# Kernel tuning notes

Hardware: AMD Instinct MI355X
Metric: run time of the kernel (lower is better)

Reference implementation:

```python
import jax, jax.numpy as jnp
import numpy as np

NOISE_WEIGHT = 1.0
CHAMFER_WEIGHT = 0.1
CHUNK = 1024


def _min_dist_chunked(a, b):
    """For each point in a [B,N,3], squared distance to nearest point in b [B,M,3].
    Processed in chunks of CHUNK points of `a` to avoid materializing [B,N,M].
    Returns [B,N]."""
    B, N, _ = a.shape
    b_sq = jnp.sum(b * b, axis=-1)  # [B,M]
    nc = N // CHUNK
    a_chunks = jnp.moveaxis(a.reshape(B, nc, CHUNK, 3), 1, 0)  # [nc,B,CHUNK,3]

    def body(carry, a_c):
        a_sq = jnp.sum(a_c * a_c, axis=-1)  # [B,CHUNK]
        # d[b,i,j] = |a_i|^2 + |b_j|^2 - 2 a_i.b_j
        d = a_sq[:, :, None] + b_sq[:, None, :] - 2.0 * jnp.einsum('bid,bjd->bij', a_c, b)
        d = jnp.maximum(d, 0.0)
        return carry, jnp.min(d, axis=2)  # [B,CHUNK]

    _, mins = jax.lax.scan(body, None, a_chunks)  # [nc,B,CHUNK]
    return jnp.moveaxis(mins, 0, 1).reshape(B, N)


def chamfer_distance(pred, target):
    d_pt = _min_dist_chunked(pred, target)   # [B,N]
    d_tp = _min_dist_chunked(target, pred)   # [B,M]
    return jnp.mean(d_pt, axis=1) + jnp.mean(d_tp, axis=1)  # [B]


def setup_inputs() -> dict:
    key = jax.random.key(0)
    k1, k2, k3, k4 = jax.random.split(key, 4)
    B, N = 8, 16384
    return {
        'predicted_noise': jax.random.normal(k1, (B, N, 3), dtype=jnp.float32),
        'actual_noise': jax.random.normal(k2, (B, N, 3), dtype=jnp.float32),
        'predicted_points_coarse': jax.random.normal(k3, (B, N, 3), dtype=jnp.float32),
        'target_points_coarse': jax.random.normal(k4, (B, N, 3), dtype=jnp.float32),
    }


def reference(predicted_noise, actual_noise, predicted_points_coarse, target_points_coarse):
    noise_loss = jnp.mean(jnp.abs(predicted_noise - actual_noise))
    chamfer_loss = jnp.mean(chamfer_distance(predicted_points_coarse, target_points_coarse))
    total_loss = NOISE_WEIGHT * noise_loss + CHAMFER_WEIGHT * chamfer_loss
    return total_loss
```

## Files before the change

kernel.cpp:

```cpp
#include <hip/hip_runtime.h>
#include <stdint.h>

#define NPTS        16384
#define BATCH       8
#define QPB         128
#define QBLKS       (NPTS / QPB)
#define CHAM_BLOCKS (BATCH * 2 * QBLKS)
#define NOISE_N     (BATCH * NPTS * 3)
#define NOISE_V4    (NOISE_N / 4)
#define NPTS_TOT    (BATCH * NPTS)
#define PACK_BLOCKS (NPTS_TOT / 256)
#define REF_ITERS   (NPTS * 8 / 1024)

#define WS_NOISE_PART 0
#define WS_CHAM_PART  4096
#define WS_PK_PRED    16384
#define WS_PK_TARG    (WS_PK_PRED + 8 * NPTS_TOT)
#define WS_R_PRED     (WS_PK_TARG + 8 * NPTS_TOT)
#define WS_R_TARG     (WS_R_PRED + 4 * NPTS_TOT)

using halfx4 = __attribute__((ext_vector_type(4))) _Float16;
using intx4  = __attribute__((ext_vector_type(4))) int;

__device__ __forceinline__ unsigned int f2h(float f) {
  union { _Float16 h; unsigned short s; } v; v.h = (_Float16)f; return v.s;
}
__device__ __forceinline__ float h2f(unsigned short s) {
  union { _Float16 h; unsigned short u; } v; v.u = s; return (float)v.h;
}

__device__ __forceinline__ void mfma_min(halfx4 a, halfx4 b, float& acc) {
  asm("v_mfma_f32_32x32x8_f16 v[48:63], %1, %2, 0\n\t"
      "s_nop 7\n\t"
      "s_nop 7\n\t"
      "s_nop 1\n\t"
      "v_min3_f32 v48, v48, v49, v50\n\t"
      "v_min3_f32 v51, v51, v52, v53\n\t"
      "v_min3_f32 v54, v54, v55, v56\n\t"
      "v_min3_f32 v57, v57, v58, v59\n\t"
      "v_min3_f32 v60, v60, v61, v62\n\t"
      "v_min3_f32 v48, v48, v51, v54\n\t"
      "v_min3_f32 v57, v57, v60, v63\n\t"
      "v_min3_f32 %0, %0, v48, v57"
      : "+v"(acc)
      : "v"(a), "v"(b)
      : "v48","v49","v50","v51","v52","v53","v54","v55",
        "v56","v57","v58","v59","v60","v61","v62","v63");
}

__global__ void pack_noise_kernel(const float* __restrict__ pred,
                                  const float* __restrict__ targ,
                                  const float4* __restrict__ na,
                                  const float4* __restrict__ nb,
                                  ushort4* __restrict__ pk_pred,
                                  ushort4* __restrict__ pk_targ,
                                  float* __restrict__ r_pred,
                                  float* __restrict__ r_targ,
                                  float* __restrict__ part) {
  int i = blockIdx.x * 256 + threadIdx.x;
  {
    float x = pred[3*i+0], y = pred[3*i+1], z = pred[3*i+2];
    float s = __builtin_fmaf(x, x, __builtin_fmaf(y, y, z*z));
    pk_pred[i] = make_ushort4((unsigned short)f2h(x), (unsigned short)f2h(y),
                              (unsigned short)f2h(z), (unsigned short)f2h(s));
    r_pred[i] = s;
  }
  {
    float x = targ[3*i+0], y = targ[3*i+1], z = targ[3*i+2];
    float s = __builtin_fmaf(x, x, __builtin_fmaf(y, y, z*z));
    pk_targ[i] = make_ushort4((unsigned short)f2h(x), (unsigned short)f2h(y),
                              (unsigned short)f2h(z), (unsigned short)f2h(s));
    r_targ[i] = s;
  }
  float sn = 0.f;
  if (i < NOISE_V4) {
    float4 pa = na[i], pb = nb[i];
    sn = fabsf(pa.x-pb.x) + fabsf(pa.y-pb.y) + fabsf(pa.z-pb.z) + fabsf(pa.w-pb.w);
  }
  for (int o = 1; o < 64; o <<= 1) sn += __shfl_xor(sn, o);
  __shared__ float ws4[4];
  int lane = threadIdx.x & 63, wv = threadIdx.x >> 6;
  if (lane == 0) ws4[wv] = sn;
  __syncthreads();
  if (threadIdx.x == 0) part[blockIdx.x] = ws4[0] + ws4[1] + ws4[2] + ws4[3];
}

__global__ __launch_bounds__(256, 8)
void chamfer_kernel(const ushort4* __restrict__ pk_pred,
                    const ushort4* __restrict__ pk_targ,
                    const float* __restrict__ r_pred,
                    const float* __restrict__ r_targ,
                    float* __restrict__ part) {
  __shared__ float wsum[4];

  const int tid  = threadIdx.x;
  const int lane = tid & 63;
  const int wv   = tid >> 6;
  const int col  = lane & 31;

  const int blk  = blockIdx.x;
  const int qblk = blk & (QBLKS - 1);
  const int bd   = blk >> 7;
  const int dir  = bd & 1;
  const int b    = bd >> 1;

  const ushort4* qpk = dir ? pk_targ : pk_pred;
  const float*   qr  = dir ? r_targ  : r_pred;
  const ushort4* ref = dir ? pk_pred : pk_targ;
  qpk += b * NPTS; qr += b * NPTS; ref += b * NPTS;

  const int q = qblk * QPB + wv * 32 + col;
  ushort4 qt = qpk[q];
  unsigned int nx = f2h(-2.f * h2f(qt.x));
  unsigned int ny = f2h(-2.f * h2f(qt.y));
  unsigned int nz = f2h(-2.f * h2f(qt.z));
  unsigned int lo = (ny << 16) | nx;
  unsigned int hi = (0x3C00u << 16) | nz;
  const bool hh = (lane >= 32);

  union BF { halfx4 v; unsigned int u[2]; };
  BF fb0, fb1;
  fb0.u[0] = hh ? 0u : lo; fb0.u[1] = hh ? 0u : hi;
  fb1.u[0] = hh ? lo : 0u; fb1.u[1] = hh ? hi : 0u;

  union AF { intx4 i; halfx4 h[2]; };

  const char* rbase = (const char*)ref + lane * 16;
  float m0 = 1e30f, m1 = 1e30f, m2 = 1e30f, m3 = 1e30f;

  intx4 pA = *(const intx4*)(rbase + 0 * 1024);
  intx4 pB = *(const intx4*)(rbase + 1 * 1024);
  intx4 pC = *(const intx4*)(rbase + 2 * 1024);
  intx4 pD = *(const intx4*)(rbase + 3 * 1024);

#define STEP(P, k)                                                          \
  {                                                                         \
    AF fa; fa.i = P;                                                        \
    P = *(const intx4*)(rbase + (size_t)(((it + (k) + 4) & (REF_ITERS - 1)) * 1024)); \
    mfma_min(fa.h[0], fb0.v, m0);                                           \
    mfma_min(fa.h[0], fb1.v, m1);                                           \
    mfma_min(fa.h[1], fb0.v, m2);                                           \
    mfma_min(fa.h[1], fb1.v, m3);                                           \
  }

  for (int it = 0; it < REF_ITERS; it += 4) {
    STEP(pA, 0)
    STEP(pB, 1)
    STEP(pC, 2)
    STEP(pD, 3)
  }
#undef STEP

  float m = fminf(fminf(m0, m1), fminf(m2, m3));

  m = fminf(m, __shfl_xor(m, 32));
  float rq = qr[q];
  float dmin = fmaxf(rq + m, 0.f);
  float v = (lane < 32) ? dmin : 0.f;
  for (int o = 1; o < 32; o <<= 1) v += __shfl_xor(v, o);
  if (lane == 0) wsum[wv] = v;
  __syncthreads();
  if (tid == 0) part[blockIdx.x] = wsum[0] + wsum[1] + wsum[2] + wsum[3];
}

__global__ void final_kernel(const float* __restrict__ part_noise,
                             const float* __restrict__ part_cham,
                             float* __restrict__ out) {
  __shared__ float red[256];
  float s = 0.f;
  for (int i = threadIdx.x; i < PACK_BLOCKS; i += 256) s += part_noise[i];
  float t = 0.f;
  for (int i = threadIdx.x; i < CHAM_BLOCKS; i += 256) t += part_cham[i];
  red[threadIdx.x] = s; __syncthreads();
  for (int o = 128; o; o >>= 1) { if (threadIdx.x < o) red[threadIdx.x] += red[threadIdx.x + o]; __syncthreads(); }
  float noise_sum = red[0];
  __syncthreads();
  red[threadIdx.x] = t; __syncthreads();
  for (int o = 128; o; o >>= 1) { if (threadIdx.x < o) red[threadIdx.x] += red[threadIdx.x + o]; __syncthreads(); }
  if (threadIdx.x == 0)
    out[0] = noise_sum * (1.f / NOISE_N) + 0.1f * red[0] * (1.f / NPTS_TOT);
}

extern "C" void kernel_launch(void* const* d_in, const int* in_sizes, int n_in,
                              void* d_out, int out_size, void* d_ws, size_t ws_size,
                              hipStream_t stream) {
  const float* pn = (const float*)d_in[0];
  const float* an = (const float*)d_in[1];
  const float* pp = (const float*)d_in[2];
  const float* tp = (const float*)d_in[3];

  char* ws = (char*)d_ws;
  float*   noise_part = (float*)(ws + WS_NOISE_PART);
  float*   cham_part  = (float*)(ws + WS_CHAM_PART);
  ushort4* pk_pred    = (ushort4*)(ws + WS_PK_PRED);
  ushort4* pk_targ    = (ushort4*)(ws + WS_PK_TARG);
  float*   r_pred     = (float*)(ws + WS_R_PRED);
  float*   r_targ     = (float*)(ws + WS_R_TARG);

  pack_noise_kernel<<<PACK_BLOCKS, 256, 0, stream>>>(pp, tp, (const float4*)pn, (const float4*)an,
                                                     pk_pred, pk_targ, r_pred, r_targ, noise_part);
  chamfer_kernel<<<CHAM_BLOCKS, 256, 0, stream>>>(pk_pred, pk_targ, r_pred, r_targ, cham_part);
  final_kernel<<<1, 256, 0, stream>>>(noise_part, cham_part, (float*)d_out);
}
```

Baseline: 170.4 us.

## Interleave MFMA pairs with min reductions and fold final reduction into chamfer kernel

Replaces the per-MFMA inline asm, which waited out each matrix op's latency with s_nops, with a grouped asm block. It issues two MFMAs into separate accumulator banks and runs the min3 reduction of one while the next MFMA executes, hiding MFMA latency. It also removes the separate final reduction kernel: the last chamfer block, found via an atomic ticket, sums the partials and writes the output. This drops one launch but adds an atomic, a fence and a serial tail in one block, and uses more clobbered VGPRs, which may lower occupancy.

Result: slower. 293.8 us (+72.4%).

```diff
diff --git a/kernel.cpp b/kernel.cpp
--- a/kernel.cpp
+++ b/kernel.cpp
@@ -14,6 +14,7 @@
 
 #define WS_NOISE_PART 0
 #define WS_CHAM_PART  4096
+#define WS_TICKET     12288
 #define WS_PK_PRED    16384
 #define WS_PK_TARG    (WS_PK_PRED + 8 * NPTS_TOT)
 #define WS_R_PRED     (WS_PK_TARG + 8 * NPTS_TOT)
@@ -29,10 +30,40 @@
   union { _Float16 h; unsigned short u; } v; v.u = s; return (float)v.h;
 }
 
-__device__ __forceinline__ void mfma_min(halfx4 a, halfx4 b, float& acc) {
-  asm("v_mfma_f32_32x32x8_f16 v[48:63], %1, %2, 0\n\t"
+__device__ __forceinline__ void mfma_group(halfx4 a0, halfx4 a1, halfx4 b0, halfx4 b1,
+                                           float& m0, float& m1, float& m2, float& m3) {
+  asm("s_nop 1\n\t"
+      "v_mfma_f32_32x32x8_f16 v[32:47], %4, %6, 0\n\t"
+      "v_mfma_f32_32x32x8_f16 v[48:63], %4, %7, 0\n\t"
       "s_nop 7\n\t"
       "s_nop 7\n\t"
+      "v_min3_f32 v32, v32, v33, v34\n\t"
+      "v_min3_f32 v35, v35, v36, v37\n\t"
+      "v_min3_f32 v38, v38, v39, v40\n\t"
+      "v_min3_f32 v41, v41, v42, v43\n\t"
+      "v_min3_f32 v44, v44, v45, v46\n\t"
+      "v_min3_f32 v32, v32, v35, v38\n\t"
+      "v_min3_f32 v41, v41, v44, v47\n\t"
+      "v_min3_f32 %0, %0, v32, v41\n\t"
+      "v_mfma_f32_32x32x8_f16 v[32:47], %5, %6, 0\n\t"
+      "v_min3_f32 v48, v48, v49, v50\n\t"
+      "v_min3_f32 v51, v51, v52, v53\n\t"
+      "v_min3_f32 v54, v54, v55, v56\n\t"
+      "v_min3_f32 v57, v57, v58, v59\n\t"
+      "v_min3_f32 v60, v60, v61, v62\n\t"
+      "v_min3_f32 v48, v48, v51, v54\n\t"
+      "v_min3_f32 v57, v57, v60, v63\n\t"
+      "v_min3_f32 %1, %1, v48, v57\n\t"
+      "v_mfma_f32_32x32x8_f16 v[48:63], %5, %7, 0\n\t"
+      "s_nop 0\n\t"
+      "v_min3_f32 v32, v32, v33, v34\n\t"
+      "v_min3_f32 v35, v35, v36, v37\n\t"
+      "v_min3_f32 v38, v38, v39, v40\n\t"
+      "v_min3_f32 v41, v41, v42, v43\n\t"
+      "v_min3_f32 v44, v44, v45, v46\n\t"
+      "v_min3_f32 v32, v32, v35, v38\n\t"
+      "v_min3_f32 v41, v41, v44, v47\n\t"
+      "v_min3_f32 %2, %2, v32, v41\n\t"
       "s_nop 1\n\t"
       "v_min3_f32 v48, v48, v49, v50\n\t"
       "v_min3_f32 v51, v51, v52, v53\n\t"
@@ -41,10 +72,12 @@
       "v_min3_f32 v60, v60, v61, v62\n\t"
       "v_min3_f32 v48, v48, v51, v54\n\t"
       "v_min3_f32 v57, v57, v60, v63\n\t"
-      "v_min3_f32 %0, %0, v48, v57"
-      : "+v"(acc)
-      : "v"(a), "v"(b)
-      : "v48","v49","v50","v51","v52","v53","v54","v55",
+      "v_min3_f32 %3, %3, v48, v57"
+      : "+v"(m0), "+v"(m1), "+v"(m2), "+v"(m3)
+      : "v"(a0), "v"(a1), "v"(b0), "v"(b1)
+      : "v32","v33","v34","v35","v36","v37","v38","v39",
+        "v40","v41","v42","v43","v44","v45","v46","v47",
+        "v48","v49","v50","v51","v52","v53","v54","v55",
         "v56","v57","v58","v59","v60","v61","v62","v63");
 }
 
@@ -56,8 +89,10 @@
                                   ushort4* __restrict__ pk_targ,
                                   float* __restrict__ r_pred,
                                   float* __restrict__ r_targ,
-                                  float* __restrict__ part) {
+                                  float* __restrict__ part,
+                                  unsigned int* __restrict__ ticket) {
   int i = blockIdx.x * 256 + threadIdx.x;
+  if (i == 0) *ticket = 0u;
   {
     float x = pred[3*i+0], y = pred[3*i+1], z = pred[3*i+2];
     float s = __builtin_fmaf(x, x, __builtin_fmaf(y, y, z*z));
@@ -90,8 +125,12 @@
                     const ushort4* __restrict__ pk_targ,
                     const float* __restrict__ r_pred,
                     const float* __restrict__ r_targ,
-                    float* __restrict__ part) {
+                    float* __restrict__ part,
+                    const float* __restrict__ part_noise,
+                    unsigned int* __restrict__ ticket,
+                    float* __restrict__ out) {
   __shared__ float wsum[4];
+  __shared__ float flagv;
 
   const int tid  = threadIdx.x;
   const int lane = tid & 63;
@@ -130,26 +169,19 @@
 
   intx4 pA = *(const intx4*)(rbase + 0 * 1024);
   intx4 pB = *(const intx4*)(rbase + 1 * 1024);
-  intx4 pC = *(const intx4*)(rbase + 2 * 1024);
-  intx4 pD = *(const intx4*)(rbase + 3 * 1024);
-
-#define STEP(P, k)                                                          \
-  {                                                                         \
-    AF fa; fa.i = P;                                                        \
-    P = *(const intx4*)(rbase + (size_t)(((it + (k) + 4) & (REF_ITERS - 1)) * 1024)); \
-    mfma_min(fa.h[0], fb0.v, m0);                                           \
-    mfma_min(fa.h[0], fb1.v, m1);                                           \
-    mfma_min(fa.h[1], fb0.v, m2);                                           \
-    mfma_min(fa.h[1], fb1.v, m3);                                           \
-  }
-
-  for (int it = 0; it < REF_ITERS; it += 4) {
-    STEP(pA, 0)
-    STEP(pB, 1)
-    STEP(pC, 2)
-    STEP(pD, 3)
-  }
-#undef STEP
+
+  for (int it = 0; it < REF_ITERS; it += 2) {
+    {
+      AF fa; fa.i = pA;
+      pA = *(const intx4*)(rbase + (size_t)(((it + 2) & (REF_ITERS - 1)) * 1024));
+      mfma_group(fa.h[0], fa.h[1], fb0.v, fb1.v, m0, m1, m2, m3);
+    }
+    {
+      AF fa; fa.i = pB;
+      pB = *(const intx4*)(rbase + (size_t)(((it + 3) & (REF_ITERS - 1)) * 1024));
+      mfma_group(fa.h[0], fa.h[1], fb0.v, fb1.v, m0, m1, m2, m3);
+    }
+  }
 
   float m = fminf(fminf(m0, m1), fminf(m2, m3));
 
@@ -160,25 +192,27 @@
   for (int o = 1; o < 32; o <<= 1) v += __shfl_xor(v, o);
   if (lane == 0) wsum[wv] = v;
   __syncthreads();
-  if (tid == 0) part[blockIdx.x] = wsum[0] + wsum[1] + wsum[2] + wsum[3];
-}
-
-__global__ void final_kernel(const float* __restrict__ part_noise,
-                             const float* __restrict__ part_cham,
-                             float* __restrict__ out) {
-  __shared__ float red[256];
-  float s = 0.f;
-  for (int i = threadIdx.x; i < PACK_BLOCKS; i += 256) s += part_noise[i];
-  float t = 0.f;
-  for (int i = threadIdx.x; i < CHAM_BLOCKS; i += 256) t += part_cham[i];
-  red[threadIdx.x] = s; __syncthreads();
-  for (int o = 128; o; o >>= 1) { if (threadIdx.x < o) red[threadIdx.x] += red[threadIdx.x + o]; __syncthreads(); }
-  float noise_sum = red[0];
+
+  if (tid == 0) {
+    atomicExch(&part[blk], wsum[0] + wsum[1] + wsum[2] + wsum[3]);
+    __threadfence();
+    unsigned int t = atomicAdd(ticket, 1u);
+    flagv = (t == CHAM_BLOCKS - 1) ? 1.f : 0.f;
+  }
   __syncthreads();
-  red[threadIdx.x] = t; __syncthreads();
-  for (int o = 128; o; o >>= 1) { if (threadIdx.x < o) red[threadIdx.x] += red[threadIdx.x + o]; __syncthreads(); }
-  if (threadIdx.x == 0)
-    out[0] = noise_sum * (1.f / NOISE_N) + 0.1f * red[0] * (1.f / NPTS_TOT);
+
+  if (flagv != 0.f) {
+    float s = 0.f;
+    for (int i = tid; i < PACK_BLOCKS; i += 256) s += part_noise[i];
+    float c = 0.f;
+    for (int i = tid; i < CHAM_BLOCKS; i += 256) c += atomicAdd(&part[i], 0.f);
+    float acc = s * (1.f / NOISE_N) + 0.1f * c * (1.f / NPTS_TOT);
+    for (int o = 1; o < 64; o <<= 1) acc += __shfl_xor(acc, o);
+    __syncthreads();
+    if (lane == 0) wsum[wv] = acc;
+    __syncthreads();
+    if (tid == 0) out[0] = wsum[0] + wsum[1] + wsum[2] + wsum[3];
+  }
 }
 
 extern "C" void kernel_launch(void* const* d_in, const int* in_sizes, int n_in,
@@ -190,15 +224,17 @@
   const float* tp = (const float*)d_in[3];
 
   char* ws = (char*)d_ws;
-  float*   noise_part = (float*)(ws + WS_NOISE_PART);
-  float*   cham_part  = (float*)(ws + WS_CHAM_PART);
-  ushort4* pk_pred    = (ushort4*)(ws + WS_PK_PRED);
-  ushort4* pk_targ    = (ushort4*)(ws + WS_PK_TARG);
-  float*   r_pred     = (float*)(ws + WS_R_PRED);
-  float*   r_targ     = (float*)(ws + WS_R_TARG);
+  float*        noise_part = (float*)(ws + WS_NOISE_PART);
+  float*        cham_part  = (float*)(ws + WS_CHAM_PART);
+  unsigned int* ticket     = (unsigned int*)(ws + WS_TICKET);
+  ushort4*      pk_pred    = (ushort4*)(ws + WS_PK_PRED);
+  ushort4*      pk_targ    = (ushort4*)(ws + WS_PK_TARG);
+  float*        r_pred     = (float*)(ws + WS_R_PRED);
+  float*        r_targ     = (float*)(ws + WS_R_TARG);
 
   pack_noise_kernel<<<PACK_BLOCKS, 256, 0, stream>>>(pp, tp, (const float4*)pn, (const float4*)an,
-                                                     pk_pred, pk_targ, r_pred, r_targ, noise_part);
-  chamfer_kernel<<<CHAM_BLOCKS, 256, 0, stream>>>(pk_pred, pk_targ, r_pred, r_targ, cham_part);
-  final_kernel<<<1, 256, 0, stream>>>(noise_part, cham_part, (float*)d_out);
-}
+                                                     pk_pred, pk_targ, r_pred, r_targ,
+                                                     noise_part, ticket);
+  chamfer_kernel<<<CHAM_BLOCKS, 256, 0, stream>>>(pk_pred, pk_targ, r_pred, r_targ,
+                                                  cham_part, noise_part, ticket, (float*)d_out);
+}
```
